# Kernel optimization log

Hardware: AMD Instinct MI355X
Metric: run time of the kernel (lower is better)

## Reference

```python
import jax, jax.numpy as jnp
import numpy as np

H = 64  # GRU hidden size (hard-coded in module)


def _gru_scan(x_proj, w_hh, b_hh):
    """Run a single-direction GRU (torch gate order r,z,n).

    x_proj: [T, B, 3H] precomputed input projections (x @ W_ih^T + b_ih)
    w_hh:   [3H, H], b_hh: [3H]
    Returns all hidden states [T, B, H].
    """
    w_hr, w_hz, w_hn = w_hh[:H], w_hh[H:2 * H], w_hh[2 * H:]
    b_hr, b_hz, b_hn = b_hh[:H], b_hh[H:2 * H], b_hh[2 * H:]
    B = x_proj.shape[1]
    h0 = jnp.zeros((B, H), dtype=x_proj.dtype)

    def step(h, xp):
        xr, xz, xn = xp[:, :H], xp[:, H:2 * H], xp[:, 2 * H:]
        r = jax.nn.sigmoid(xr + h @ w_hr.T + b_hr)
        z = jax.nn.sigmoid(xz + h @ w_hz.T + b_hz)
        n = jnp.tanh(xn + r * (h @ w_hn.T + b_hn))
        h_new = (1.0 - z) * n + z * h
        return h_new, h_new

    _, hs = jax.lax.scan(step, h0, x_proj)
    return hs  # [T, B, H]


def setup_inputs() -> dict:
    key = jax.random.key(0)
    ks = jax.random.split(key, 11)
    B, T, D = 512, 512, 32
    s_ih = 1.0 / np.sqrt(H)
    u = lambda k, shape: jax.random.uniform(k, shape, jnp.float32, -s_ih, s_ih)
    return {
        "x": jax.random.normal(ks[0], (B, T, D), dtype=jnp.float32),
        # forward direction GRU params
        "w_ih_f": u(ks[1], (3 * H, D)),
        "w_hh_f": u(ks[2], (3 * H, H)),
        "b_ih_f": u(ks[3], (3 * H,)),
        "b_hh_f": u(ks[4], (3 * H,)),
        # backward direction GRU params
        "w_ih_b": u(ks[5], (3 * H, D)),
        "w_hh_b": u(ks[6], (3 * H, H)),
        "b_ih_b": u(ks[7], (3 * H,)),
        "b_hh_b": u(ks[8], (3 * H,)),
        # fc head: Linear(128,64) -> LeakyReLU(0.2) -> Linear(64,1)
        "fc1_w": jax.random.normal(ks[9], (64, 2 * H), dtype=jnp.float32) * (1.0 / np.sqrt(2 * H)),
        "fc1_b": jnp.zeros((64,), dtype=jnp.float32),
        "fc2_w": jax.random.normal(ks[10], (1, 64), dtype=jnp.float32) * (1.0 / np.sqrt(64)),
        "fc2_b": jnp.zeros((1,), dtype=jnp.float32),
    }


def reference(x, w_ih_f, w_hh_f, b_ih_f, b_hh_f,
              w_ih_b, w_hh_b, b_ih_b, b_hh_b,
              fc1_w, fc1_b, fc2_w, fc2_b):
    # x: [B, T, D] -> time-major [T, B, D]
    xt = jnp.swapaxes(x, 0, 1)
    # precompute input projections for all timesteps (one big GEMM per dir)
    xp_f = jnp.einsum('tbd,gd->tbg', xt, w_ih_f) + b_ih_f  # [T,B,3H]
    xp_b = jnp.einsum('tbd,gd->tbg', xt, w_ih_b) + b_ih_b

    hs_f = _gru_scan(xp_f, w_hh_f, b_hh_f)            # forward over t=0..T-1
    hs_b = _gru_scan(xp_b[::-1], w_hh_b, b_hh_b)      # backward: reversed time
    # out[:, -1, :] = concat(fwd hidden at t=T-1, bwd hidden at t=T-1).
    # bwd hidden at original t=T-1 is the FIRST step of the reversed scan.
    last = jnp.concatenate([hs_f[-1], hs_b[0]], axis=-1)  # [B, 2H]

    h1 = last @ fc1_w.T + fc1_b
    h1 = jnp.where(h1 >= 0, h1, 0.2 * h1)  # LeakyReLU(0.2)
    return h1 @ fc2_w.T + fc2_b  # [B, 1]
```

## Files before the change

### kernel.cpp

```cpp
#include <hip/hip_runtime.h>


namespace {
constexpr int T = 512;
constexpr int BATCH = 512;
constexpr int D = 32;
constexpr int H = 64;
constexpr int THREADS = 128;
}

typedef float v2f __attribute__((ext_vector_type(2)));

__device__ __forceinline__ float rcpf(float x) { return __builtin_amdgcn_rcpf(x); }
__device__ __forceinline__ float sigm(float x) { return rcpf(1.0f + __expf(-x)); }
__device__ __forceinline__ float tanh_fast(float x) {
    return 1.0f - 2.0f * rcpf(__expf(2.0f * x) + 1.0f);
}

__device__ __forceinline__ void pk2(v2f& acc, v2f w, v2f v) {
    asm("v_pk_fma_f32 %0, %1, %2, %0" : "+v"(acc) : "v"(w), "v"(v));
}

__device__ __forceinline__ float pair_sum(float v) {
    int i = __builtin_bit_cast(int, v);
    float t = __builtin_bit_cast(float,
        __builtin_amdgcn_update_dpp(0, i, 0xB1, 0xF, 0xF, true));
    return v + t;
}

__global__ __launch_bounds__(THREADS, 1) void gru_fused_kernel(
    const float* __restrict__ x,
    const float* __restrict__ w_ih_f, const float* __restrict__ w_hh_f,
    const float* __restrict__ b_ih_f, const float* __restrict__ b_hh_f,
    const float* __restrict__ w_ih_b, const float* __restrict__ b_ih_b,
    const float* __restrict__ b_hh_b,
    const float* __restrict__ fc1_w, const float* __restrict__ fc1_b,
    const float* __restrict__ fc2_w, const float* __restrict__ fc2_b,
    float* __restrict__ out)
{
    const int b   = blockIdx.x;
    const int tid = threadIdx.x;
    const int j   = tid >> 1;
    const int q   = tid & 1;
    const int kh0 = q * 32;
    const int kx0 = q * 16;

    __shared__ v2f x_lds[T * D / 2];
    __shared__ __align__(16) float h_lds[2][H];
    __shared__ float last_lds[2 * H];

    v2f wr2[16], wz2[16], wn2[16], ur2[8], uz2[8], un2[8];
    {
        const v2f* pr = reinterpret_cast<const v2f*>(w_hh_f + (size_t)j * H + kh0);
        const v2f* pz = reinterpret_cast<const v2f*>(w_hh_f + (size_t)(H + j) * H + kh0);
        const v2f* pn = reinterpret_cast<const v2f*>(w_hh_f + (size_t)(2 * H + j) * H + kh0);
        #pragma unroll
        for (int m = 0; m < 16; ++m) { wr2[m] = pr[m]; wz2[m] = pz[m]; wn2[m] = pn[m]; }
        const v2f* qr = reinterpret_cast<const v2f*>(w_ih_f + (size_t)j * D + kx0);
        const v2f* qz = reinterpret_cast<const v2f*>(w_ih_f + (size_t)(H + j) * D + kx0);
        const v2f* qn = reinterpret_cast<const v2f*>(w_ih_f + (size_t)(2 * H + j) * D + kx0);
        #pragma unroll
        for (int m = 0; m < 8; ++m) { ur2[m] = qr[m]; uz2[m] = qz[m]; un2[m] = qn[m]; }
    }

    const float pre_r  = b_ih_f[j]         + b_hh_f[j];
    const float pre_z  = b_ih_f[H + j]     + b_hh_f[H + j];
    const float pre_nx = b_ih_f[2 * H + j];
    const float pre_nh = b_hh_f[2 * H + j];

    {
        const float4* xg  = reinterpret_cast<const float4*>(x + (size_t)b * T * D);
        float4*       xl4 = reinterpret_cast<float4*>(x_lds);
        #pragma unroll 4
        for (int i = tid; i < T * D / 4; i += THREADS) xl4[i] = xg[i];
    }
    if (tid < H) h_lds[0][tid] = 0.0f;
    __syncthreads();

    v2f axr = {0.f, 0.f}, axz = {0.f, 0.f}, axn = {0.f, 0.f};
    {
        const v2f* xt2 = x_lds + q * 8;
        #pragma unroll
        for (int m = 0; m < 8; ++m) {
            v2f xv = xt2[m];
            pk2(axr, ur2[m], xv);
            pk2(axz, uz2[m], xv);
            pk2(axn, un2[m], xv);
        }
    }

    float hold = 0.0f;

    for (int t = 0; t < T; ++t) {
        const int cur = t & 1, nxt = cur ^ 1;

        v2f hh[16];
        {
            const v2f* hp = reinterpret_cast<const v2f*>(&h_lds[cur][kh0]);
            #pragma unroll
            for (int m = 0; m < 16; ++m) hh[m] = hp[m];
        }

        v2f pr = axr, pz = axz, nh = {0.f, 0.f};
        #pragma unroll
        for (int m = 0; m < 16; ++m) pk2(pr, wr2[m], hh[m]);
        #pragma unroll
        for (int m = 0; m < 16; ++m) pk2(pz, wz2[m], hh[m]);
        #pragma unroll
        for (int m = 0; m < 16; ++m) pk2(nh, wn2[m], hh[m]);
        const v2f axn_t = axn;

        {
            const int tn = (t + 1) & (T - 1);
            const v2f* xt2 = x_lds + tn * (D / 2) + q * 8;
            axr = {0.f, 0.f}; axz = {0.f, 0.f}; axn = {0.f, 0.f};
            #pragma unroll
            for (int m = 0; m < 8; ++m) {
                v2f xv = xt2[m];
                pk2(axr, ur2[m], xv);
                pk2(axz, uz2[m], xv);
                pk2(axn, un2[m], xv);
            }
        }

        const float vr  = pair_sum(pr.x + pr.y);
        const float vz  = pair_sum(pz.x + pz.y);
        const float vnh = pair_sum(nh.x + nh.y);
        const float vnx = pair_sum(axn_t.x + axn_t.y);

        const float r = sigm(vr + pre_r);
        const float z = sigm(vz + pre_z);
        const float n = tanh_fast(vnx + pre_nx + r * (vnh + pre_nh));
        const float hnew = n + z * (hold - n);
        hold = hnew;
        if (q == 0) h_lds[nxt][j] = hnew;
        __syncthreads();
    }

    const int wave = tid >> 6, lane = tid & 63;

    if (wave == 0) last_lds[lane] = h_lds[T & 1][lane];

    if (wave == 1) {
        const float* xT = reinterpret_cast<const float*>(x_lds) + (T - 1) * D;
        const int jj = lane;
        float xr = b_ih_b[jj];
        float xz = b_ih_b[H + jj];
        float xn = b_ih_b[2 * H + jj];
        #pragma unroll
        for (int k = 0; k < D; ++k) {
            const float xv = xT[k];
            xr = fmaf(w_ih_b[(size_t)jj * D + k],           xv, xr);
            xz = fmaf(w_ih_b[(size_t)(H + jj) * D + k],     xv, xz);
            xn = fmaf(w_ih_b[(size_t)(2 * H + jj) * D + k], xv, xn);
        }
        const float r = sigm(xr + b_hh_b[jj]);
        const float z = sigm(xz + b_hh_b[H + jj]);
        const float n = tanh_fast(xn + r * b_hh_b[2 * H + jj]);
        last_lds[H + jj] = (1.0f - z) * n;
    }
    __syncthreads();

    if (wave == 0) {
        float acc = fc1_b[lane];
        const float* w1 = fc1_w + (size_t)lane * (2 * H);
        #pragma unroll 8
        for (int c = 0; c < 2 * H; ++c) acc = fmaf(w1[c], last_lds[c], acc);
        acc = (acc >= 0.0f) ? acc : 0.2f * acc;
        float red = acc * fc2_w[lane];
        #pragma unroll
        for (int off = 32; off > 0; off >>= 1)
            red += __shfl_down(red, off);
        if (lane == 0) out[b] = red + fc2_b[0];
    }
}

extern "C" void kernel_launch(void* const* d_in, const int* in_sizes, int n_in,
                              void* d_out, int out_size, void* d_ws, size_t ws_size,
                              hipStream_t stream) {
    const float* x      = (const float*)d_in[0];
    const float* w_ih_f = (const float*)d_in[1];
    const float* w_hh_f = (const float*)d_in[2];
    const float* b_ih_f = (const float*)d_in[3];
    const float* b_hh_f = (const float*)d_in[4];
    const float* w_ih_b = (const float*)d_in[5];
    const float* b_ih_b = (const float*)d_in[7];
    const float* b_hh_b = (const float*)d_in[8];
    const float* fc1_w  = (const float*)d_in[9];
    const float* fc1_b  = (const float*)d_in[10];
    const float* fc2_w  = (const float*)d_in[11];
    const float* fc2_b  = (const float*)d_in[12];
    float* out = (float*)d_out;

    gru_fused_kernel<<<BATCH, THREADS, 0, stream>>>(
        x, w_ih_f, w_hh_f, b_ih_f, b_hh_f,
        w_ih_b, b_ih_b, b_hh_b,
        fc1_w, fc1_b, fc2_w, fc2_b, out);
}
```

Baseline: 202.3 us.

## Unroll GRU recurrence by two with x prefetch and lightweight LDS barrier

Unrolls the time loop by two with ping-pong register sets so the x row for step t+2 is loaded from LDS one step ahead and its input projection is computed from registers, taking LDS reads off the critical path. Replaces __syncthreads with an explicit lgkmcnt wait plus s_barrier, and lets both lanes of each pair write h (same value) to drop the branch. The aim is to shorten per-step latency of the serial recurrence, at the cost of more registers for the prefetched x values.

```diff
diff --git a/kernel.cpp b/kernel.cpp
--- a/kernel.cpp
+++ b/kernel.cpp
@@ -1,5 +1,4 @@
 #include <hip/hip_runtime.h>
-
 
 namespace {
 constexpr int T = 512;
@@ -26,6 +25,11 @@
     float t = __builtin_bit_cast(float,
         __builtin_amdgcn_update_dpp(0, i, 0xB1, 0xF, 0xF, true));
     return v + t;
+}
+
+__device__ __forceinline__ void lds_barrier() {
+    asm volatile("s_waitcnt lgkmcnt(0)" ::: "memory");
+    __builtin_amdgcn_s_barrier();
 }
 
 __global__ __launch_bounds__(THREADS, 1) void gru_fused_kernel(
@@ -77,65 +81,71 @@
     if (tid < H) h_lds[0][tid] = 0.0f;
     __syncthreads();
 
-    v2f axr = {0.f, 0.f}, axz = {0.f, 0.f}, axn = {0.f, 0.f};
+    v2f axrA = {0.f,0.f}, axzA = {0.f,0.f}, axnA = {0.f,0.f};
     {
         const v2f* xt2 = x_lds + q * 8;
         #pragma unroll
         for (int m = 0; m < 8; ++m) {
             v2f xv = xt2[m];
-            pk2(axr, ur2[m], xv);
-            pk2(axz, uz2[m], xv);
-            pk2(axn, un2[m], xv);
+            pk2(axrA, ur2[m], xv); pk2(axzA, uz2[m], xv); pk2(axnA, un2[m], xv);
         }
     }
+    v2f xvA[8];
+    {
+        const v2f* xt2 = x_lds + (D / 2) + q * 8;
+        #pragma unroll
+        for (int m = 0; m < 8; ++m) xvA[m] = xt2[m];
+    }
+    v2f axrB, axzB, axnB;
+    v2f xvB[8];
 
     float hold = 0.0f;
 
-    for (int t = 0; t < T; ++t) {
-        const int cur = t & 1, nxt = cur ^ 1;
-
-        v2f hh[16];
-        {
-            const v2f* hp = reinterpret_cast<const v2f*>(&h_lds[cur][kh0]);
-            #pragma unroll
-            for (int m = 0; m < 16; ++m) hh[m] = hp[m];
-        }
-
-        v2f pr = axr, pz = axz, nh = {0.f, 0.f};
-        #pragma unroll
-        for (int m = 0; m < 16; ++m) pk2(pr, wr2[m], hh[m]);
-        #pragma unroll
-        for (int m = 0; m < 16; ++m) pk2(pz, wz2[m], hh[m]);
-        #pragma unroll
-        for (int m = 0; m < 16; ++m) pk2(nh, wn2[m], hh[m]);
-        const v2f axn_t = axn;
-
-        {
-            const int tn = (t + 1) & (T - 1);
-            const v2f* xt2 = x_lds + tn * (D / 2) + q * 8;
-            axr = {0.f, 0.f}; axz = {0.f, 0.f}; axn = {0.f, 0.f};
-            #pragma unroll
-            for (int m = 0; m < 8; ++m) {
-                v2f xv = xt2[m];
-                pk2(axr, ur2[m], xv);
-                pk2(axz, uz2[m], xv);
-                pk2(axn, un2[m], xv);
-            }
-        }
-
-        const float vr  = pair_sum(pr.x + pr.y);
-        const float vz  = pair_sum(pz.x + pz.y);
-        const float vnh = pair_sum(nh.x + nh.y);
-        const float vnx = pair_sum(axn_t.x + axn_t.y);
-
-        const float r = sigm(vr + pre_r);
-        const float z = sigm(vz + pre_z);
-        const float n = tanh_fast(vnx + pre_nx + r * (vnh + pre_nh));
-        const float hnew = n + z * (hold - n);
-        hold = hnew;
-        if (q == 0) h_lds[nxt][j] = hnew;
-        __syncthreads();
-    }
+    #define GRU_STEP(CUR, NXT, AXR,AXZ,AXN, XV, AXR2,AXZ2,AXN2, XV2, T2)       \
+    {                                                                          \
+        v2f hh[16];                                                            \
+        {                                                                      \
+            const v2f* hp = reinterpret_cast<const v2f*>(&h_lds[CUR][kh0]);    \
+            _Pragma("unroll")                                                  \
+            for (int m = 0; m < 16; ++m) hh[m] = hp[m];                        \
+        }                                                                      \
+        {                                                                      \
+            const v2f* xt2 = x_lds + (size_t)((T2) & (T - 1)) * (D / 2) + q * 8;\
+            _Pragma("unroll")                                                  \
+            for (int m = 0; m < 8; ++m) XV2[m] = xt2[m];                       \
+        }                                                                      \
+        AXR2 = {0.f,0.f}; AXZ2 = {0.f,0.f}; AXN2 = {0.f,0.f};                  \
+        _Pragma("unroll")                                                      \
+        for (int m = 0; m < 8; ++m) {                                          \
+            pk2(AXR2, ur2[m], XV[m]);                                          \
+            pk2(AXZ2, uz2[m], XV[m]);                                          \
+            pk2(AXN2, un2[m], XV[m]);                                          \
+        }                                                                      \
+        v2f pr = AXR, pz = AXZ, nh = {0.f,0.f};                                \
+        _Pragma("unroll")                                                      \
+        for (int m = 0; m < 16; ++m) pk2(pr, wr2[m], hh[m]);                   \
+        _Pragma("unroll")                                                      \
+        for (int m = 0; m < 16; ++m) pk2(pz, wz2[m], hh[m]);                   \
+        _Pragma("unroll")                                                      \
+        for (int m = 0; m < 16; ++m) pk2(nh, wn2[m], hh[m]);                   \
+        const float vr = pair_sum(pr.x + pr.y);                                \
+        const float r  = sigm(vr + pre_r);            \
+        const float vz  = pair_sum(pz.x + pz.y);                               \
+        const float vnh = pair_sum(nh.x + nh.y);                               \
+        const float vnx = pair_sum(AXN.x + AXN.y);                             \
+        const float z  = sigm(vz + pre_z);                                     \
+        const float n  = tanh_fast(vnx + pre_nx + r * (vnh + pre_nh));         \
+        const float hnew = n + z * (hold - n);            \
+        hold = hnew;                                                           \
+        h_lds[NXT][j] = hnew;            \
+        lds_barrier();                                                         \
+    }
+
+    for (int t = 0; t < T; t += 2) {
+        GRU_STEP(0, 1, axrA, axzA, axnA, xvA, axrB, axzB, axnB, xvB, t + 2)
+        GRU_STEP(1, 0, axrB, axzB, axnB, xvB, axrA, axzA, axnA, xvA, t + 3)
+    }
+    #undef GRU_STEP
 
     const int wave = tid >> 6, lane = tid & 63;
 
```

Result: faster. 191.1 us (-5.5%).
